# Kernel optimization log

Hardware: AMD Instinct MI355X
Metric: run time of the kernel (lower is better)

Reference implementation:

```python
import jax, jax.numpy as jnp
import numpy as np
from jax import lax

EPS = 1e-5
ENC_CH = [3, 64, 128, 256, 512]
DEC_CH = [512, 256, 128, 64, 3]

def setup_inputs() -> dict:
    key = jax.random.key(0)
    ks = iter(jax.random.split(key, 64))
    d = {}
    d['x'] = jax.random.normal(next(ks), (16, 3, 256, 256), jnp.float32)
    for i in range(4):
        ci, co = ENC_CH[i], ENC_CH[i + 1]
        d[f'enc_w{i}'] = jax.random.normal(next(ks), (co, ci, 3, 3), jnp.float32) / np.sqrt(ci * 9.0).astype(np.float32)
        d[f'enc_b{i}'] = jnp.zeros((co,), jnp.float32)
        d[f'enc_g{i}'] = jnp.ones((co,), jnp.float32)
        d[f'enc_be{i}'] = jnp.zeros((co,), jnp.float32)
    for i in range(4):
        ci, co = DEC_CH[i], DEC_CH[i + 1]
        # torch ConvTranspose2d weight layout: (in, out, kh, kw)
        d[f'dec_w{i}'] = jax.random.normal(next(ks), (ci, co, 3, 3), jnp.float32) / np.sqrt(ci * 9.0).astype(np.float32)
        d[f'dec_b{i}'] = jnp.zeros((co,), jnp.float32)
        d[f'dec_g{i}'] = jnp.ones((co,), jnp.float32)
        d[f'dec_be{i}'] = jnp.zeros((co,), jnp.float32)
    n_emb = 2048
    d['emb'] = jax.random.uniform(next(ks), (n_emb, 512), jnp.float32, minval=-1.0 / n_emb, maxval=1.0 / n_emb)
    return d

def _bn(x, g, b):
    # training-mode batchnorm (biased variance over N,H,W), matching nn.BatchNorm2d default state
    m = jnp.mean(x, (0, 2, 3), keepdims=True)
    v = jnp.mean((x - m) ** 2, (0, 2, 3), keepdims=True)
    return g[None, :, None, None] * (x - m) * lax.rsqrt(v + EPS) + b[None, :, None, None]

def _enc_block(x, w, b, g, be):
    y = lax.conv_general_dilated(x, w, (2, 2), ((1, 1), (1, 1)), dimension_numbers=('NCHW', 'OIHW', 'NCHW'))
    y = y + b[None, :, None, None]
    return jax.nn.gelu(_bn(y, g, be), approximate=False)

def _dec_block(x, w, b, g, be):
    # ConvTranspose2d(k=3, s=2, p=1, output_padding=1): lhs_dilation=2, pad (1,2), flipped kernel
    w2 = jnp.flip(w, (2, 3)).transpose(1, 0, 2, 3)  # (out, in, 3, 3)
    y = lax.conv_general_dilated(x, w2, (1, 1), ((1, 2), (1, 2)), lhs_dilation=(2, 2), dimension_numbers=('NCHW', 'OIHW', 'NCHW'))
    y = y + b[None, :, None, None]
    return jax.nn.gelu(_bn(y, g, be), approximate=False)

def _forward(x, enc_p, dec_p, emb):
    h = x
    for (w, b, g, be) in enc_p:
        h = _enc_block(h, w, b, g, be)
    # --- VectorQuantizer ---
    B, C, H, W = h.shape
    f = h.transpose(0, 2, 3, 1).reshape(B, H * W, C)  # (b, hw, c)
    # squared distances via expansion (same math as broadcasted diff-sum, minus the 34GB intermediate)
    d2 = jnp.sum(f * f, -1, keepdims=True) - 2.0 * jnp.einsum('bnc,ec->bne', f, emb) + jnp.sum(emb * emb, -1)[None, None, :]
    idx = jnp.argmin(d2, -1)  # (b, hw)
    e = emb[idx]  # (b, hw, c)
    e = e.transpose(0, 2, 1).reshape(B, C, H, W)
    sg = lax.stop_gradient
    loss = jnp.mean((h - sg(e)) ** 2) + 0.25 * jnp.mean((sg(h) - e) ** 2)
    # NOTE: original forward returns x (encoder output), NOT the quantized emb_x — faithful to source
    y = h
    for (w, b, g, be) in dec_p:
        y = _dec_block(y, w, b, g, be)
    return jnp.tanh(y), loss

def reference(x, enc_w0, enc_b0, enc_g0, enc_be0, enc_w1, enc_b1, enc_g1, enc_be1, enc_w2, enc_b2, enc_g2, enc_be2, enc_w3, enc_b3, enc_g3, enc_be3, dec_w0, dec_b0, dec_g0, dec_be0, dec_w1, dec_b1, dec_g1, dec_be1, dec_w2, dec_b2, dec_g2, dec_be2, dec_w3, dec_b3, dec_g3, dec_be3, emb):
    enc_p = [(enc_w0, enc_b0, enc_g0, enc_be0), (enc_w1, enc_b1, enc_g1, enc_be1), (enc_w2, enc_b2, enc_g2, enc_be2), (enc_w3, enc_b3, enc_g3, enc_be3)]
    dec_p = [(dec_w0, dec_b0, dec_g0, dec_be0), (dec_w1, dec_b1, dec_g1, dec_be1), (dec_w2, dec_b2, dec_g2, dec_be2), (dec_w3, dec_b3, dec_g3, dec_be3)]
    return _forward(x, enc_p, dec_p, emb)
```

## Files before the change

kernel.cpp:

```cpp
#include <hip/hip_runtime.h>
#include <math.h>

typedef _Float16 half8 __attribute__((ext_vector_type(8)));
typedef _Float16 half4t __attribute__((ext_vector_type(4)));
typedef float floatx4 __attribute__((ext_vector_type(4)));

struct ConvDesc {
  int HI, WI;
  int CIs;
  int OYs, OXs;
  int SXY;
  int osxy;
  int HO, WO;
  int CO_pad, CO_real, CO_store;
  int nclass;
  int py[4], px[4], nt[4];
  int tt[4][9], tdy[4][9], tdx[4][9];
};

#define STAT_SLOTS 16

template<int BM, int BN>
__global__ __launch_bounds__(256) void conv_gemm(
    const _Float16* __restrict__ act, const _Float16* __restrict__ wB,
    const float* __restrict__ bias, _Float16* __restrict__ y,
    float* __restrict__ stats, ConvDesc d)
{
  constexpr int WM = BM / 2, WN = BN / 2, FM = WM / 16, FN = WN / 16;
  constexpr int ARPT = BM / 64, BT = BN / 64;
  constexpr int AP = BM * 8 + 8;
  constexpr int ASZ = 4 * AP;
  constexpr int BSZ = BT * 2048;
  __shared__ __align__(16) _Float16 As[2 * ASZ];
  __shared__ __align__(16) _Float16 Bs[2 * BSZ];

  const int tid = threadIdx.x;
  const int cls = blockIdx.z;
  const int m0 = blockIdx.x * BM, n0 = blockIdx.y * BN;
  const int q = tid & 3, r0 = tid >> 2;

  int aih[ARPT], aiw[ARPT], abase[ARPT];
  #pragma unroll
  for (int i = 0; i < ARPT; i++) {
    int p = m0 + r0 + i * 64;
    int n  = p >> (d.OYs + d.OXs);
    int oy = (p >> d.OXs) & ((1 << d.OYs) - 1);
    int ox = p & ((1 << d.OXs) - 1);
    aih[i] = oy * d.SXY;
    aiw[i] = ox * d.SXY;
    abase[i] = n * d.HI;
  }

  floatx4 acc[FM][FN] = {};
  const int wv = tid >> 6, lane = tid & 63;
  const int wm = wv >> 1, wn = wv & 1;
  const int fr = lane >> 4, fc = lane & 15;
  const int c5s = d.CIs - 5;
  const int c5m = (1 << c5s) - 1;
  const int kiters = d.nt[cls] << c5s;

  auto stageK = [&](int kk, int buf) {
    int ti = kk >> c5s, c5 = kk & c5m;
    int dy = d.tdy[cls][ti], dx = d.tdx[cls][ti];
    int kt0 = d.tt[cls][ti] << c5s;
    int c0 = c5 << 5;
    #pragma unroll
    for (int i = 0; i < ARPT; i++) {
      int ih = aih[i] + dy, iw = aiw[i] + dx;
      half8 v = {};
      if ((unsigned)ih < (unsigned)d.HI && (unsigned)iw < (unsigned)d.WI)
        v = *(const half8*)(act + ((((size_t)(abase[i] + ih)) * d.WI + iw) << d.CIs) + c0 + q * 8);
      *(half8*)(As + buf * ASZ + q * AP + (r0 + i * 64) * 8) = v;
    }
    #pragma unroll
    for (int j = 0; j < BT; j++) {
      const _Float16* src = wB + (size_t)((kt0 + c5) * (d.CO_pad >> 6) + (n0 >> 6) + j) * 2048 + tid * 8;
      *(half8*)(Bs + buf * BSZ + j * 2048 + tid * 8) = *(const half8*)src;
    }
  };

  stageK(0, 0);
  for (int kk = 0; kk < kiters; kk++) {
    __syncthreads();
    if (kk + 1 < kiters) stageK(kk + 1, (kk + 1) & 1);
    const int buf = kk & 1;
    half8 af[FM], bf[FN];
    #pragma unroll
    for (int a = 0; a < FM; a++)
      af[a] = *(const half8*)(As + buf * ASZ + fr * AP + (wm * WM + a * 16 + fc) * 8);
    #pragma unroll
    for (int b = 0; b < FN; b++) {
      int col = wn * WN + b * 16 + fc;
      bf[b] = *(const half8*)(Bs + buf * BSZ + (col >> 6) * 2048 + fr * 512 + (col & 63) * 8);
    }
    #pragma unroll
    for (int a = 0; a < FM; a++)
      #pragma unroll
      for (int b = 0; b < FN; b++)
        acc[a][b] = __builtin_amdgcn_mfma_f32_16x16x32_f16(af[a], bf[b], acc[a][b], 0, 0, 0);
  }

  float bv[FN];
  int colg[FN];
  #pragma unroll
  for (int b = 0; b < FN; b++) {
    int col = n0 + wn * WN + b * 16 + fc;
    colg[b] = col;
    bv[b] = (col < d.CO_real) ? bias[col] : 0.f;
  }
  float ssum[FN] = {}, ssq[FN] = {};
  const int pyc = d.py[cls], pxc = d.px[cls];
  #pragma unroll
  for (int a = 0; a < FM; a++) {
    #pragma unroll
    for (int rr = 0; rr < 4; rr++) {
      int m = m0 + wm * WM + a * 16 + fr * 4 + rr;
      int n  = m >> (d.OYs + d.OXs);
      int oy = (m >> d.OXs) & ((1 << d.OYs) - 1);
      int ox = m & ((1 << d.OXs) - 1);
      size_t opix = ((size_t)(n * d.HO + oy * d.osxy + pyc)) * d.WO + ox * d.osxy + pxc;
      _Float16* dst = y + opix * d.CO_store;
      #pragma unroll
      for (int b = 0; b < FN; b++) {
        float val = acc[a][b][rr] + bv[b];
        if (colg[b] < d.CO_store) dst[colg[b]] = (_Float16)val;
        ssum[b] += val; ssq[b] += val * val;
      }
    }
  }

  __syncthreads();
  float2* red = (float2*)As;
  #pragma unroll
  for (int b = 0; b < FN; b++)
    red[(wn * WN + b * 16 + fc) * 8 + wm * 4 + fr] = make_float2(ssum[b], ssq[b]);
  __syncthreads();
  if (tid < BN) {
    float s = 0.f, qv = 0.f;
    #pragma unroll
    for (int g2 = 0; g2 < 8; g2++) { float2 v = red[tid * 8 + g2]; s += v.x; qv += v.y; }
    int slot = (blockIdx.x + blockIdx.z) & (STAT_SLOTS - 1);
    float* sp = stats + ((size_t)(n0 + tid) * STAT_SLOTS + slot) * 2;
    atomicAdd(sp, s); atomicAdd(sp + 1, qv);
  }
}

__global__ __launch_bounds__(256) void dec3_fused(
    const _Float16* __restrict__ act, const _Float16* __restrict__ wB,
    const float* __restrict__ bias, _Float16* __restrict__ y,
    float* __restrict__ stats)
{
  __shared__ __align__(16) _Float16 As[4 * 3168];
  __shared__ __align__(16) _Float16 Bs[9216];
  const int tid = threadIdx.x;
  const int n = blockIdx.x >> 6;
  const int y0 = (blockIdx.x & 63) << 1;
  const int wv = tid >> 6, lane = tid & 63;
  const int fr = lane >> 4, fc = lane & 15;

  for (int i = tid; i < 1152; i += 256)
    *(half8*)(Bs + i * 8) = *(const half8*)(wB + i * 8);

  floatx4 acc[4][4] = {};

  for (int c5 = 0; c5 < 2; c5++) {
    __syncthreads();
    for (int i = tid; i < 1584; i += 256) {
      int slot = i >> 2, q = i & 3;
      int prow = slot / 132, pcol = slot - prow * 132;
      int row = y0 + prow;
      half8 v = {};
      if (row < 128 && pcol < 128)
        v = *(const half8*)(act + (((size_t)(n * 128 + row)) * 128 + pcol) * 64 + c5 * 32 + q * 8);
      *(half8*)(As + q * 3168 + slot * 8) = v;
    }
    __syncthreads();
    #pragma unroll
    for (int t = 0; t < 9; t++) {
      const int ky = t / 3, kx = t % 3;
      const int dy = (ky == 0) ? 1 : 0, dx = (kx == 0) ? 1 : 0;
      const int cls = ((ky + 1) & 1) * 2 + ((kx + 1) & 1);
      half8 bf = *(const half8*)(Bs + (t * 2 + c5) * 512 + fr * 128 + fc * 8);
      #pragma unroll
      for (int a = 0; a < 4; a++) {
        int m = wv * 64 + a * 16 + fc;
        int r = m >> 7, xx = m & 127;
        half8 af = *(const half8*)(As + fr * 3168 + ((r + dy) * 132 + xx + dx) * 8);
        acc[cls][a] = __builtin_amdgcn_mfma_f32_16x16x32_f16(af, bf, acc[cls][a], 0, 0, 0);
      }
    }
  }

  float bv = (fc < 3) ? bias[fc] : 0.f;
  float s4 = 0.f, q4 = 0.f;
  if (fc < 4) {
    #pragma unroll
    for (int cls = 0; cls < 4; cls++) {
      int py = cls >> 1, px = cls & 1;
      #pragma unroll
      for (int a = 0; a < 4; a++) {
        #pragma unroll
        for (int rr = 0; rr < 4; rr++) {
          int m = wv * 64 + a * 16 + fr * 4 + rr;
          int r = m >> 7, xx = m & 127;
          size_t opix = ((size_t)(n * 256 + (y0 + r) * 2 + py)) * 256 + xx * 2 + px;
          float val = acc[cls][a][rr] + bv;
          y[opix * 4 + fc] = (_Float16)val;
          s4 += val; q4 += val * val;
        }
      }
    }
  }
  __syncthreads();
  float2* red = (float2*)As;
  if (fc < 4) red[fc * 16 + wv * 4 + fr] = make_float2(s4, q4);
  __syncthreads();
  if (tid < 4) {
    float s = 0.f, qv = 0.f;
    #pragma unroll
    for (int g2 = 0; g2 < 16; g2++) { float2 v = red[tid * 16 + g2]; s += v.x; qv += v.y; }
    int slot = blockIdx.x & (STAT_SLOTS - 1);
    float* sp = stats + ((size_t)tid * STAT_SLOTS + slot) * 2;
    atomicAdd(sp, s); atomicAdd(sp + 1, qv);
  }
}

__global__ __launch_bounds__(256) void vq_gemm(const _Float16* __restrict__ h,
    const _Float16* __restrict__ embB, const float* __restrict__ ee,
    float* __restrict__ minval, int* __restrict__ minidx)
{
  __shared__ char smem[32768];
  _Float16* As = (_Float16*)smem;
  _Float16* Bs = (_Float16*)(smem + 8448);
  const int tid = threadIdx.x;
  const int m0 = blockIdx.x * 128, n0 = blockIdx.y * 128;
  const int q = tid & 3, r0 = tid >> 2;
  floatx4 acc[4][4] = {};
  const int wv = tid >> 6, lane = tid & 63;
  const int wm = wv >> 1, wn = wv & 1;
  const int fr = lane >> 4, fc = lane & 15;

  for (int c5 = 0; c5 < 16; c5++) {
    #pragma unroll
    for (int i = 0; i < 2; i++) {
      half8 v = *(const half8*)(h + (size_t)(m0 + r0 + i * 64) * 512 + c5 * 32 + q * 8);
      *(half8*)(As + q * 1032 + (r0 + i * 64) * 8) = v;
    }
    #pragma unroll
    for (int j = 0; j < 2; j++)
      *(half8*)(Bs + j * 2048 + tid * 8) =
          *(const half8*)(embB + (size_t)(c5 * 32 + (n0 >> 6) + j) * 2048 + tid * 8);
    __syncthreads();
    half8 af[4], bf[4];
    #pragma unroll
    for (int a = 0; a < 4; a++)
      af[a] = *(const half8*)(As + fr * 1032 + (wm * 64 + a * 16 + fc) * 8);
    #pragma unroll
    for (int b = 0; b < 4; b++) {
      int col = wn * 64 + b * 16 + fc;
      bf[b] = *(const half8*)(Bs + (col >> 6) * 2048 + fr * 512 + (col & 63) * 8);
    }
    #pragma unroll
    for (int a = 0; a < 4; a++)
      #pragma unroll
      for (int b = 0; b < 4; b++)
        acc[a][b] = __builtin_amdgcn_mfma_f32_16x16x32_f16(af[a], bf[b], acc[a][b], 0, 0, 0);
    __syncthreads();
  }

  float* sval = (float*)smem;
  int*   sidx = (int*)(smem + 16384);
  #pragma unroll
  for (int a = 0; a < 4; a++) {
    #pragma unroll
    for (int rr = 0; rr < 4; rr++) {
      int rb = wm * 64 + a * 16 + fr * 4 + rr;
      float best = 1e30f; int bi = 0;
      #pragma unroll
      for (int b = 0; b < 4; b++) {
        int e = n0 + wn * 64 + b * 16 + fc;
        float s = ee[e] - 2.f * acc[a][b][rr];
        if (s < best) { best = s; bi = e; }
      }
      sval[rb * 32 + wn * 16 + fc] = best;
      sidx[rb * 32 + wn * 16 + fc] = bi;
    }
  }
  __syncthreads();
  if (tid < 128) {
    float best = sval[tid * 32]; int bi = sidx[tid * 32];
    for (int t = 1; t < 32; t++) {
      float v = sval[tid * 32 + t]; int ix = sidx[tid * 32 + t];
      if (v < best || (v == best && ix < bi)) { best = v; bi = ix; }
    }
    minval[(size_t)(m0 + tid) * 16 + blockIdx.y] = best;
    minidx[(size_t)(m0 + tid) * 16 + blockIdx.y] = bi;
  }
}

__global__ __launch_bounds__(256) void vq_finalize(const _Float16* __restrict__ h,
    const float* __restrict__ emb, const float* __restrict__ minval,
    const int* __restrict__ minidx, float* __restrict__ lossacc)
{
  const int tid = threadIdx.x;
  const int g = tid >> 4, l = tid & 15;
  const int v = blockIdx.x * 16 + g;
  float val = minval[(size_t)v * 16 + l];
  int   idx = minidx[(size_t)v * 16 + l];
  #pragma unroll
  for (int o = 8; o > 0; o >>= 1) {
    float v2 = __shfl_down(val, o, 16);
    int   i2 = __shfl_down(idx, o, 16);
    if (v2 < val || (v2 == val && i2 < idx)) { val = v2; idx = i2; }
  }
  idx = __shfl(idx, 0, 16);
  float s = 0.f;
  #pragma unroll
  for (int j = 0; j < 32; j++) {
    int c = l + 16 * j;
    float f = (float)h[(size_t)v * 512 + c];
    float e = emb[(size_t)idx * 512 + c];
    float dd = f - e;
    s += dd * dd;
  }
  #pragma unroll
  for (int o = 8; o > 0; o >>= 1) s += __shfl_down(s, o, 16);
  if (l == 0) atomicAdd(lossacc, s);
}

__global__ __launch_bounds__(256) void bn_apply_inline(_Float16* __restrict__ y,
    const float2* __restrict__ stats, const float* __restrict__ g,
    const float* __restrict__ be, int Cs, int n8, float invM)
{
  const int C = 1 << Cs;
  __shared__ float scs[512], shs[512];
  for (int c = threadIdx.x; c < C; c += 256) {
    float s = 0.f, qv = 0.f;
    #pragma unroll
    for (int t = 0; t < STAT_SLOTS; t++) { float2 v = stats[c * STAT_SLOTS + t]; s += v.x; qv += v.y; }
    float m = s * invM, var = qv * invM - m * m;
    float sc = g[c] * rsqrtf(var + 1e-5f);
    scs[c] = sc; shs[c] = be[c] - m * sc;
  }
  __syncthreads();
  int i = blockIdx.x * 256 + threadIdx.x;
  if (i >= n8) return;
  int c0 = (i << 3) & (C - 1);
  half8 v = *(half8*)(y + (size_t)i * 8);
  half8 o;
  #pragma unroll
  for (int j = 0; j < 8; j++) {
    float x = (float)v[j] * scs[c0 + j] + shs[c0 + j];
    o[j] = (_Float16)(0.5f * x * (1.f + erff(x * 0.70710678118654752f)));
  }
  *(half8*)(y + (size_t)i * 8) = o;
}

__global__ __launch_bounds__(256) void bn_final_inline(const _Float16* __restrict__ y,
    float* __restrict__ out, const float2* __restrict__ stats,
    const float* __restrict__ g, const float* __restrict__ be,
    const float* __restrict__ lossacc)
{
  __shared__ float scs[4], shs[4];
  if (threadIdx.x < 3) {
    int c = threadIdx.x;
    float s = 0.f, qv = 0.f;
    #pragma unroll
    for (int t = 0; t < STAT_SLOTS; t++) { float2 v = stats[c * STAT_SLOTS + t]; s += v.x; qv += v.y; }
    const float invM = 1.f / 1048576.f;
    float m = s * invM, var = qv * invM - m * m;
    float sc = g[c] * rsqrtf(var + 1e-5f);
    scs[c] = sc; shs[c] = be[c] - m * sc;
  }
  __syncthreads();
  int p = blockIdx.x * 256 + threadIdx.x;
  int n = p >> 16, hw = p & 65535;
  half4t v = *(const half4t*)(y + (size_t)p * 4);
  #pragma unroll
  for (int c = 0; c < 3; c++) {
    float x = (float)v[c] * scs[c] + shs[c];
    float gg = 0.5f * x * (1.f + erff(x * 0.70710678118654752f));
    out[(size_t)(n * 3 + c) * 65536 + hw] = tanhf(gg);
  }
  if (p == 0) out[3145728] = lossacc[0] * (1.25f / 2097152.0f);
}

__global__ __launch_bounds__(256) void im2col_enc0(const float* __restrict__ x,
                                                   _Float16* __restrict__ xp)
{
  int p = blockIdx.x * 256 + threadIdx.x;
  int n = p >> 14, oy = (p >> 7) & 127, ox = p & 127;
  const float* xb = x + (size_t)n * 3 * 65536;
  _Float16 v[32];
  #pragma unroll
  for (int k = 27; k < 32; k++) v[k] = (_Float16)0.f;
  #pragma unroll
  for (int tap = 0; tap < 9; tap++) {
    int kh = tap / 3, kw = tap - kh * 3;
    int ih = 2 * oy - 1 + kh, iw = 2 * ox - 1 + kw;
    bool ok = ((unsigned)ih < 256u) && ((unsigned)iw < 256u);
    #pragma unroll
    for (int c = 0; c < 3; c++)
      v[tap * 3 + c] = ok ? (_Float16)xb[(size_t)c * 65536 + ih * 256 + iw] : (_Float16)0.f;
  }
  _Float16* dst = xp + (size_t)p * 32;
  #pragma unroll
  for (int j = 0; j < 4; j++) *(half8*)(dst + j * 8) = *(half8*)(v + j * 8);
}

__global__ void wtrans0(const float* __restrict__ w, _Float16* __restrict__ wB)
{
  int idx = blockIdx.x * 256 + threadIdx.x;
  if (idx >= 2048) return;
  int k = idx >> 6, co = idx & 63;
  int tap = k / 3, c = k - tap * 3;
  float v = (k < 27) ? w[((size_t)co * 3 + c) * 9 + tap] : 0.f;
  int kg = (k >> 3) & 3, kj = k & 7;
  wB[kg * 512 + co * 8 + kj] = (_Float16)v;
}

__global__ void wtrans_n16_dec3(const float* __restrict__ w, _Float16* __restrict__ wB)
{
  int idx = blockIdx.x * 256 + threadIdx.x;
  if (idx >= 9216) return;
  int k = idx >> 4, co = idx & 15;
  int tap = k >> 6, ci = k & 63;
  float v = 0.f;
  if (co < 3) v = w[((size_t)ci * 3 + co) * 9 + tap];
  int kt = k >> 5, kg = (k >> 3) & 3, kj = k & 7;
  wB[(size_t)kt * 512 + kg * 128 + co * 8 + kj] = (_Float16)v;
}

__global__ __launch_bounds__(256) void wtrans(const float* __restrict__ w,
    _Float16* __restrict__ wB, int CIs, int CI_real, int COs, int CO_real, int is_dec)
{
  int idx = blockIdx.x * 256 + threadIdx.x;
  int CO_pad = 1 << COs;
  int K = 9 << CIs;
  if (idx >= K * CO_pad) return;
  int k = idx >> COs, co = idx & (CO_pad - 1);
  int tap = k >> CIs, ci = k & ((1 << CIs) - 1);
  int kh = tap / 3, kw = tap - kh * 3;
  float v = 0.f;
  if (ci < CI_real && co < CO_real)
    v = is_dec ? w[(((size_t)ci * CO_real + co) * 3 + kh) * 3 + kw]
               : w[(((size_t)co * CI_real + ci) * 3 + kh) * 3 + kw];
  int kt = k >> 5, kg = (k >> 3) & 3, kj = k & 7, jt = co >> 6, cc = co & 63;
  wB[(size_t)(kt * (CO_pad >> 6) + jt) * 2048 + kg * 512 + cc * 8 + kj] = (_Float16)v;
}

__global__ __launch_bounds__(256) void embtrans(const float* __restrict__ emb,
                                                _Float16* __restrict__ embB)
{
  int idx = blockIdx.x * 256 + threadIdx.x;
  int k = idx >> 11, e = idx & 2047;
  float v = emb[(size_t)e * 512 + k];
  int kt = k >> 5, kg = (k >> 3) & 3, kj = k & 7, jt = e >> 6, cc = e & 63;
  embB[(size_t)(kt * 32 + jt) * 2048 + kg * 512 + cc * 8 + kj] = (_Float16)v;
}

__global__ __launch_bounds__(256) void emb_norms(const float* __restrict__ emb,
                                                 float* __restrict__ ee)
{
  const int wv = threadIdx.x >> 6, lane = threadIdx.x & 63;
  const int e = blockIdx.x * 4 + wv;
  float s = 0.f;
  #pragma unroll
  for (int j = 0; j < 8; j++) { float v = emb[(size_t)e * 512 + lane + j * 64]; s += v * v; }
  for (int o = 32; o > 0; o >>= 1) s += __shfl_down(s, o);
  if (lane == 0) ee[e] = s;
}

__global__ __launch_bounds__(256) void zero_stats(float* __restrict__ p, int n)
{
  int i = blockIdx.x * 256 + threadIdx.x;
  if (i < n) p[i] = 0.f;
}

static ConvDesc enc_desc(int HI, int WI, int CIs, int CO) {
  ConvDesc d = {};
  d.HI = HI; d.WI = WI; d.CIs = CIs;
  int HO = HI / 2, WO = WI / 2;
  d.OYs = __builtin_ctz(HO); d.OXs = __builtin_ctz(WO);
  d.SXY = 2; d.osxy = 1; d.HO = HO; d.WO = WO;
  d.CO_pad = CO; d.CO_real = CO; d.CO_store = CO;
  d.nclass = 1; d.py[0] = 0; d.px[0] = 0; d.nt[0] = 9;
  for (int t = 0; t < 9; t++) { d.tt[0][t] = t; d.tdy[0][t] = t / 3 - 1; d.tdx[0][t] = t % 3 - 1; }
  return d;
}

static ConvDesc dec_desc(int HI, int WI, int CIs, int CO_pad, int CO_real, int CO_store) {
  ConvDesc d = {};
  d.HI = HI; d.WI = WI; d.CIs = CIs;
  d.OYs = __builtin_ctz(HI); d.OXs = __builtin_ctz(WI);
  d.SXY = 1; d.osxy = 2; d.HO = 2 * HI; d.WO = 2 * WI;
  d.CO_pad = CO_pad; d.CO_real = CO_real; d.CO_store = CO_store;
  d.nclass = 4;
  int kys[2][2] = {{1, -1}, {0, 2}}, dis[2][2] = {{0, -1}, {1, 0}}, cnt[2] = {1, 2};
  for (int py = 0; py < 2; py++)
    for (int px = 0; px < 2; px++) {
      int c = py * 2 + px; d.py[c] = py; d.px[c] = px;
      int m = 0;
      for (int a = 0; a < cnt[py]; a++)
        for (int b = 0; b < cnt[px]; b++) {
          d.tt[c][m] = kys[py][a] * 3 + kys[px][b];
          d.tdy[c][m] = dis[py][a]; d.tdx[c][m] = dis[px][b]; m++;
        }
      d.nt[c] = m;
    }
  return d;
}

extern "C" void kernel_launch(void* const* d_in, const int* in_sizes, int n_in,
                              void* d_out, int out_size, void* d_ws, size_t ws_size,
                              hipStream_t stream)
{
  const float* x = (const float*)d_in[0];
  const float *ew[4], *ebi[4], *eg[4], *ebe[4];
  const float *dw[4], *dbi[4], *dg[4], *dbe[4];
  for (int i = 0; i < 4; i++) {
    ew[i]  = (const float*)d_in[1 + 4 * i];
    ebi[i] = (const float*)d_in[2 + 4 * i];
    eg[i]  = (const float*)d_in[3 + 4 * i];
    ebe[i] = (const float*)d_in[4 + 4 * i];
    dw[i]  = (const float*)d_in[17 + 4 * i];
    dbi[i] = (const float*)d_in[18 + 4 * i];
    dg[i]  = (const float*)d_in[19 + 4 * i];
    dbe[i] = (const float*)d_in[20 + 4 * i];
  }
  const float* emb = (const float*)d_in[33];
  float* out = (float*)d_out;
  _Float16* wsh = (_Float16*)d_ws;

  _Float16* bufA = wsh;
  _Float16* xp   = wsh;
  _Float16* bufB = wsh + 33554432;
  size_t wboff = 50331648;
  _Float16* wbE[4], *wbD[4];
  size_t wbsz[8] = {18432, 73728, 294912, 1179648, 1179648, 294912, 73728, 36864};
  for (int i = 0; i < 4; i++) { wbE[i] = wsh + wboff; wboff += wbsz[i]; }
  for (int i = 0; i < 4; i++) { wbD[i] = wsh + wboff; wboff += wbsz[4 + i]; }
  _Float16* embB = wsh + wboff;
  float* f32 = (float*)(wsh + 54532096);
  float* statsAll = f32;
  float* lossacc  = f32 + 131072;
  float* ee       = f32 + 131080;
  float* minval   = f32 + 133128;
  int*   minidx   = (int*)(f32 + 198664);
  auto statsL = [&](int i) { return statsAll + (size_t)i * 16384; };

  zero_stats<<<513, 256, 0, stream>>>(statsAll, 131073);
  im2col_enc0<<<1024, 256, 0, stream>>>(x, xp);
  wtrans0<<<8, 256, 0, stream>>>(ew[0], wbE[0]);
  wtrans<<<288, 256, 0, stream>>>(ew[1], wbE[1], 6, 64, 7, 128, 0);
  wtrans<<<1152, 256, 0, stream>>>(ew[2], wbE[2], 7, 128, 8, 256, 0);
  wtrans<<<4608, 256, 0, stream>>>(ew[3], wbE[3], 8, 256, 9, 512, 0);
  wtrans<<<4608, 256, 0, stream>>>(dw[0], wbD[0], 9, 512, 8, 256, 1);
  wtrans<<<1152, 256, 0, stream>>>(dw[1], wbD[1], 8, 256, 7, 128, 1);
  wtrans<<<288, 256, 0, stream>>>(dw[2], wbD[2], 7, 128, 6, 64, 1);
  wtrans_n16_dec3<<<36, 256, 0, stream>>>(dw[3], wbD[3]);
  embtrans<<<4096, 256, 0, stream>>>(emb, embB);
  emb_norms<<<512, 256, 0, stream>>>(emb, ee);

  {
    ConvDesc d = {};
    d.HI = 512; d.WI = 512; d.CIs = 5; d.OYs = 9; d.OXs = 9; d.SXY = 1; d.osxy = 1;
    d.HO = 512; d.WO = 512; d.CO_pad = 64; d.CO_real = 64; d.CO_store = 64;
    d.nclass = 1; d.nt[0] = 1;
    conv_gemm<128, 64><<<dim3(2048, 1, 1), 256, 0, stream>>>(xp, wbE[0], ebi[0], bufB, statsL(0), d);
    bn_apply_inline<<<8192, 256, 0, stream>>>(bufB, (const float2*)statsL(0), eg[0], ebe[0], 6, 2097152, 1.f / 262144.f);
  }
  {
    ConvDesc d = enc_desc(128, 128, 6, 128);
    conv_gemm<128, 128><<<dim3(512, 1, 1), 256, 0, stream>>>(bufB, wbE[1], ebi[1], bufA, statsL(1), d);
    bn_apply_inline<<<4096, 256, 0, stream>>>(bufA, (const float2*)statsL(1), eg[1], ebe[1], 7, 1048576, 1.f / 65536.f);
  }
  {
    ConvDesc d = enc_desc(64, 64, 7, 256);
    conv_gemm<128, 64><<<dim3(128, 4, 1), 256, 0, stream>>>(bufA, wbE[2], ebi[2], bufB, statsL(2), d);
    bn_apply_inline<<<2048, 256, 0, stream>>>(bufB, (const float2*)statsL(2), eg[2], ebe[2], 8, 524288, 1.f / 16384.f);
  }
  {
    ConvDesc d = enc_desc(32, 32, 8, 512);
    conv_gemm<64, 64><<<dim3(64, 8, 1), 256, 0, stream>>>(bufB, wbE[3], ebi[3], bufA, statsL(3), d);
    bn_apply_inline<<<1024, 256, 0, stream>>>(bufA, (const float2*)statsL(3), eg[3], ebe[3], 9, 262144, 1.f / 4096.f);
  }
  _Float16* h = bufA;

  vq_gemm<<<dim3(32, 16), 256, 0, stream>>>(h, embB, ee, minval, minidx);
  vq_finalize<<<256, 256, 0, stream>>>(h, emb, minval, minidx, lossacc);

  {
    ConvDesc d = dec_desc(16, 16, 9, 256, 256, 256);
    conv_gemm<64, 64><<<dim3(64, 4, 4), 256, 0, stream>>>(h, wbD[0], dbi[0], bufB, statsL(4), d);
    bn_apply_inline<<<2048, 256, 0, stream>>>(bufB, (const float2*)statsL(4), dg[0], dbe[0], 8, 524288, 1.f / 16384.f);
  }
  {
    ConvDesc d = dec_desc(32, 32, 8, 128, 128, 128);
    conv_gemm<128, 128><<<dim3(128, 1, 4), 256, 0, stream>>>(bufB, wbD[1], dbi[1], bufA, statsL(5), d);
    bn_apply_inline<<<4096, 256, 0, stream>>>(bufA, (const float2*)statsL(5), dg[1], dbe[1], 7, 1048576, 1.f / 65536.f);
  }
  {
    ConvDesc d = dec_desc(64, 64, 7, 64, 64, 64);
    conv_gemm<128, 64><<<dim3(512, 1, 4), 256, 0, stream>>>(bufA, wbD[2], dbi[2], bufB, statsL(6), d);
    bn_apply_inline<<<8192, 256, 0, stream>>>(bufB, (const float2*)statsL(6), dg[2], dbe[2], 6, 2097152, 1.f / 262144.f);
  }
  {
    dec3_fused<<<1024, 256, 0, stream>>>(bufB, wbD[3], dbi[3], bufA, statsL(7));
    bn_final_inline<<<4096, 256, 0, stream>>>(bufA, out, (const float2*)statsL(7), dg[3], dbe[3], lossacc);
  }
}
```

Before: 696.0 us.

## Merge prep kernels into one launch and add fused dec2 transposed-conv kernel

Replaces the twelve preprocessing launches (stat zeroing, im2col, weight and embedding transposes, embedding norms) with a single prep_all kernel that dispatches on block index, cutting launch overhead. It also replaces the generic 4-class conv_gemm for decoder layer 2 with a dedicated dec2_fused kernel. Each block of that kernel loads one input row pair into LDS once and computes all four output parity classes from it, reusing the input tile across classes. The risks are branch divergence in the merged prep kernel and lower occupancy from the large LDS weight buffer in dec2_fused.

```diff
diff --git a/kernel.cpp b/kernel.cpp
--- a/kernel.cpp
+++ b/kernel.cpp
@@ -145,6 +145,87 @@
   }
 }
 
+__global__ __launch_bounds__(256) void dec2_fused(
+    const _Float16* __restrict__ act, const _Float16* __restrict__ wB,
+    const float* __restrict__ bias, _Float16* __restrict__ y,
+    float* __restrict__ stats)
+{
+  __shared__ __align__(16) _Float16 As[4 * 1056];
+  __shared__ __align__(16) _Float16 Bs[18432];
+  const int tid = threadIdx.x;
+  const int n = blockIdx.x >> 6;
+  const int R = blockIdx.x & 63;
+  const int wv = tid >> 6, lane = tid & 63;
+  const int fr = lane >> 4, fc = lane & 15;
+
+  floatx4 acc[4][4] = {};
+
+  for (int c5 = 0; c5 < 4; c5++) {
+    __syncthreads();
+    for (int i = tid; i < 528; i += 256) {
+      int slot = i >> 2, q = i & 3;
+      int hr = slot / 66, hc = slot - hr * 66;
+      int grow = R + hr;
+      half8 v = {};
+      if (grow < 64 && hc < 64)
+        v = *(const half8*)(act + (((size_t)(n * 64 + grow)) * 64 + hc) * 128 + c5 * 32 + q * 8);
+      *(half8*)(As + q * 1056 + slot * 8) = v;
+    }
+    #pragma unroll
+    for (int t = 0; t < 9; t++)
+      *(half8*)(Bs + t * 2048 + tid * 8) =
+          *(const half8*)(wB + (size_t)(t * 4 + c5) * 2048 + tid * 8);
+    __syncthreads();
+    #pragma unroll
+    for (int t = 0; t < 9; t++) {
+      const int ky = t / 3, kx = t % 3;
+      const int dy = (ky == 0) ? 1 : 0, dx = (kx == 0) ? 1 : 0;
+      const int cls = ((ky + 1) & 1) * 2 + ((kx + 1) & 1);
+      half8 af = *(const half8*)(As + fr * 1056 + (dy * 66 + wv * 16 + fc + dx) * 8);
+      #pragma unroll
+      for (int b = 0; b < 4; b++) {
+        half8 bf = *(const half8*)(Bs + t * 2048 + fr * 512 + (b * 16 + fc) * 8);
+        acc[cls][b] = __builtin_amdgcn_mfma_f32_16x16x32_f16(af, bf, acc[cls][b], 0, 0, 0);
+      }
+    }
+  }
+
+  float bv[4];
+  #pragma unroll
+  for (int b = 0; b < 4; b++) bv[b] = bias[b * 16 + fc];
+  float ssum[4] = {}, ssq[4] = {};
+  #pragma unroll
+  for (int cls = 0; cls < 4; cls++) {
+    int py = cls >> 1, px = cls & 1;
+    int orow = 2 * R + py;
+    #pragma unroll
+    for (int b = 0; b < 4; b++) {
+      #pragma unroll
+      for (int rr = 0; rr < 4; rr++) {
+        int ipx = wv * 16 + fr * 4 + rr;
+        size_t opix = ((size_t)(n * 128 + orow)) * 128 + 2 * ipx + px;
+        float val = acc[cls][b][rr] + bv[b];
+        y[opix * 64 + b * 16 + fc] = (_Float16)val;
+        ssum[b] += val; ssq[b] += val * val;
+      }
+    }
+  }
+  __syncthreads();
+  float2* red = (float2*)As;
+  #pragma unroll
+  for (int b = 0; b < 4; b++)
+    red[(b * 16 + fc) * 16 + wv * 4 + fr] = make_float2(ssum[b], ssq[b]);
+  __syncthreads();
+  if (tid < 64) {
+    float s = 0.f, qv = 0.f;
+    #pragma unroll
+    for (int g2 = 0; g2 < 16; g2++) { float2 v = red[tid * 16 + g2]; s += v.x; qv += v.y; }
+    int slot = blockIdx.x & (STAT_SLOTS - 1);
+    float* sp = stats + ((size_t)tid * STAT_SLOTS + slot) * 2;
+    atomicAdd(sp, s); atomicAdd(sp + 1, qv);
+  }
+}
+
 __global__ __launch_bounds__(256) void dec3_fused(
     const _Float16* __restrict__ act, const _Float16* __restrict__ wB,
     const float* __restrict__ bias, _Float16* __restrict__ y,
@@ -385,59 +466,17 @@
   if (p == 0) out[3145728] = lossacc[0] * (1.25f / 2097152.0f);
 }
 
-__global__ __launch_bounds__(256) void im2col_enc0(const float* __restrict__ x,
-                                                   _Float16* __restrict__ xp)
-{
-  int p = blockIdx.x * 256 + threadIdx.x;
-  int n = p >> 14, oy = (p >> 7) & 127, ox = p & 127;
-  const float* xb = x + (size_t)n * 3 * 65536;
-  _Float16 v[32];
-  #pragma unroll
-  for (int k = 27; k < 32; k++) v[k] = (_Float16)0.f;
-  #pragma unroll
-  for (int tap = 0; tap < 9; tap++) {
-    int kh = tap / 3, kw = tap - kh * 3;
-    int ih = 2 * oy - 1 + kh, iw = 2 * ox - 1 + kw;
-    bool ok = ((unsigned)ih < 256u) && ((unsigned)iw < 256u);
-    #pragma unroll
-    for (int c = 0; c < 3; c++)
-      v[tap * 3 + c] = ok ? (_Float16)xb[(size_t)c * 65536 + ih * 256 + iw] : (_Float16)0.f;
-  }
-  _Float16* dst = xp + (size_t)p * 32;
-  #pragma unroll
-  for (int j = 0; j < 4; j++) *(half8*)(dst + j * 8) = *(half8*)(v + j * 8);
-}
-
-__global__ void wtrans0(const float* __restrict__ w, _Float16* __restrict__ wB)
-{
-  int idx = blockIdx.x * 256 + threadIdx.x;
-  if (idx >= 2048) return;
-  int k = idx >> 6, co = idx & 63;
-  int tap = k / 3, c = k - tap * 3;
-  float v = (k < 27) ? w[((size_t)co * 3 + c) * 9 + tap] : 0.f;
-  int kg = (k >> 3) & 3, kj = k & 7;
-  wB[kg * 512 + co * 8 + kj] = (_Float16)v;
-}
-
-__global__ void wtrans_n16_dec3(const float* __restrict__ w, _Float16* __restrict__ wB)
-{
-  int idx = blockIdx.x * 256 + threadIdx.x;
-  if (idx >= 9216) return;
-  int k = idx >> 4, co = idx & 15;
-  int tap = k >> 6, ci = k & 63;
-  float v = 0.f;
-  if (co < 3) v = w[((size_t)ci * 3 + co) * 9 + tap];
-  int kt = k >> 5, kg = (k >> 3) & 3, kj = k & 7;
-  wB[(size_t)kt * 512 + kg * 128 + co * 8 + kj] = (_Float16)v;
-}
-
-__global__ __launch_bounds__(256) void wtrans(const float* __restrict__ w,
-    _Float16* __restrict__ wB, int CIs, int CI_real, int COs, int CO_real, int is_dec)
-{
-  int idx = blockIdx.x * 256 + threadIdx.x;
+struct PrepPtrs {
+  const float *ew0, *ew1, *ew2, *ew3, *dw0, *dw1, *dw2, *dw3, *emb, *x;
+  _Float16 *wbE0, *wbE1, *wbE2, *wbE3, *wbD0, *wbD1, *wbD2, *wbD3, *embB, *xp;
+  float *ee, *stats;
+};
+
+__device__ __forceinline__ void wtrans_g(const float* __restrict__ w,
+    _Float16* __restrict__ wB, int CIs, int CI_real, int COs, int CO_real,
+    int is_dec, int idx)
+{
   int CO_pad = 1 << COs;
-  int K = 9 << CIs;
-  if (idx >= K * CO_pad) return;
   int k = idx >> COs, co = idx & (CO_pad - 1);
   int tap = k >> CIs, ci = k & ((1 << CIs) - 1);
   int kh = tap / 3, kw = tap - kh * 3;
@@ -449,32 +488,74 @@
   wB[(size_t)(kt * (CO_pad >> 6) + jt) * 2048 + kg * 512 + cc * 8 + kj] = (_Float16)v;
 }
 
-__global__ __launch_bounds__(256) void embtrans(const float* __restrict__ emb,
-                                                _Float16* __restrict__ embB)
-{
-  int idx = blockIdx.x * 256 + threadIdx.x;
-  int k = idx >> 11, e = idx & 2047;
-  float v = emb[(size_t)e * 512 + k];
-  int kt = k >> 5, kg = (k >> 3) & 3, kj = k & 7, jt = e >> 6, cc = e & 63;
-  embB[(size_t)(kt * 32 + jt) * 2048 + kg * 512 + cc * 8 + kj] = (_Float16)v;
-}
-
-__global__ __launch_bounds__(256) void emb_norms(const float* __restrict__ emb,
-                                                 float* __restrict__ ee)
-{
-  const int wv = threadIdx.x >> 6, lane = threadIdx.x & 63;
-  const int e = blockIdx.x * 4 + wv;
-  float s = 0.f;
-  #pragma unroll
-  for (int j = 0; j < 8; j++) { float v = emb[(size_t)e * 512 + lane + j * 64]; s += v * v; }
-  for (int o = 32; o > 0; o >>= 1) s += __shfl_down(s, o);
-  if (lane == 0) ee[e] = s;
-}
-
-__global__ __launch_bounds__(256) void zero_stats(float* __restrict__ p, int n)
-{
-  int i = blockIdx.x * 256 + threadIdx.x;
-  if (i < n) p[i] = 0.f;
+__global__ __launch_bounds__(256) void prep_all(PrepPtrs P)
+{
+  const int b = blockIdx.x;
+  const int tid = threadIdx.x;
+  if (b < 8) {
+    int idx = b * 256 + tid;
+    int k = idx >> 6, co = idx & 63;
+    int tap = k / 3, c = k - tap * 3;
+    float v = (k < 27) ? P.ew0[((size_t)co * 3 + c) * 9 + tap] : 0.f;
+    int kg = (k >> 3) & 3, kj = k & 7;
+    P.wbE0[kg * 512 + co * 8 + kj] = (_Float16)v;
+  } else if (b < 296) {
+    wtrans_g(P.ew1, P.wbE1, 6, 64, 7, 128, 0, (b - 8) * 256 + tid);
+  } else if (b < 1448) {
+    wtrans_g(P.ew2, P.wbE2, 7, 128, 8, 256, 0, (b - 296) * 256 + tid);
+  } else if (b < 6056) {
+    wtrans_g(P.ew3, P.wbE3, 8, 256, 9, 512, 0, (b - 1448) * 256 + tid);
+  } else if (b < 10664) {
+    wtrans_g(P.dw0, P.wbD0, 9, 512, 8, 256, 1, (b - 6056) * 256 + tid);
+  } else if (b < 11816) {
+    wtrans_g(P.dw1, P.wbD1, 8, 256, 7, 128, 1, (b - 10664) * 256 + tid);
+  } else if (b < 12104) {
+    wtrans_g(P.dw2, P.wbD2, 7, 128, 6, 64, 1, (b - 11816) * 256 + tid);
+  } else if (b < 12140) {
+    int idx = (b - 12104) * 256 + tid;
+    int k = idx >> 4, co = idx & 15;
+    int tap = k >> 6, ci = k & 63;
+    float v = 0.f;
+    if (co < 3) v = P.dw3[((size_t)ci * 3 + co) * 9 + tap];
+    int kt = k >> 5, kg = (k >> 3) & 3, kj = k & 7;
+    P.wbD3[(size_t)kt * 512 + kg * 128 + co * 8 + kj] = (_Float16)v;
+  } else if (b < 16236) {
+    int idx = (b - 12140) * 256 + tid;
+    int k = idx >> 11, e = idx & 2047;
+    float v = P.emb[(size_t)e * 512 + k];
+    int kt = k >> 5, kg = (k >> 3) & 3, kj = k & 7, jt = e >> 6, cc = e & 63;
+    P.embB[(size_t)(kt * 32 + jt) * 2048 + kg * 512 + cc * 8 + kj] = (_Float16)v;
+  } else if (b < 16749) {
+    int i = (b - 16236) * 256 + tid;
+    if (i < 131073) P.stats[i] = 0.f;
+  } else if (b < 17261) {
+    int wv = tid >> 6, lane = tid & 63;
+    int e = (b - 16749) * 4 + wv;
+    float s = 0.f;
+    #pragma unroll
+    for (int j = 0; j < 8; j++) { float v = P.emb[(size_t)e * 512 + lane + j * 64]; s += v * v; }
+    for (int o = 32; o > 0; o >>= 1) s += __shfl_down(s, o);
+    if (lane == 0) P.ee[e] = s;
+  } else {
+    int p = (b - 17261) * 256 + tid;
+    int n = p >> 14, oy = (p >> 7) & 127, ox = p & 127;
+    const float* xb = P.x + (size_t)n * 3 * 65536;
+    _Float16 v[32];
+    #pragma unroll
+    for (int k = 27; k < 32; k++) v[k] = (_Float16)0.f;
+    #pragma unroll
+    for (int tap = 0; tap < 9; tap++) {
+      int kh = tap / 3, kw = tap - kh * 3;
+      int ih = 2 * oy - 1 + kh, iw = 2 * ox - 1 + kw;
+      bool ok = ((unsigned)ih < 256u) && ((unsigned)iw < 256u);
+      #pragma unroll
+      for (int c = 0; c < 3; c++)
+        v[tap * 3 + c] = ok ? (_Float16)xb[(size_t)c * 65536 + ih * 256 + iw] : (_Float16)0.f;
+    }
+    _Float16* dst = P.xp + (size_t)p * 32;
+    #pragma unroll
+    for (int j = 0; j < 4; j++) *(half8*)(dst + j * 8) = *(half8*)(v + j * 8);
+  }
 }
 
 static ConvDesc enc_desc(int HI, int WI, int CIs, int CO) {
@@ -549,18 +630,14 @@
   int*   minidx   = (int*)(f32 + 198664);
   auto statsL = [&](int i) { return statsAll + (size_t)i * 16384; };
 
-  zero_stats<<<513, 256, 0, stream>>>(statsAll, 131073);
-  im2col_enc0<<<1024, 256, 0, stream>>>(x, xp);
-  wtrans0<<<8, 256, 0, stream>>>(ew[0], wbE[0]);
-  wtrans<<<288, 256, 0, stream>>>(ew[1], wbE[1], 6, 64, 7, 128, 0);
-  wtrans<<<1152, 256, 0, stream>>>(ew[2], wbE[2], 7, 128, 8, 256, 0);
-  wtrans<<<4608, 256, 0, stream>>>(ew[3], wbE[3], 8, 256, 9, 512, 0);
-  wtrans<<<4608, 256, 0, stream>>>(dw[0], wbD[0], 9, 512, 8, 256, 1);
-  wtrans<<<1152, 256, 0, stream>>>(dw[1], wbD[1], 8, 256, 7, 128, 1);
-  wtrans<<<288, 256, 0, stream>>>(dw[2], wbD[2], 7, 128, 6, 64, 1);
-  wtrans_n16_dec3<<<36, 256, 0, stream>>>(dw[3], wbD[3]);
-  embtrans<<<4096, 256, 0, stream>>>(emb, embB);
-  emb_norms<<<512, 256, 0, stream>>>(emb, ee);
+  PrepPtrs P;
+  P.ew0 = ew[0]; P.ew1 = ew[1]; P.ew2 = ew[2]; P.ew3 = ew[3];
+  P.dw0 = dw[0]; P.dw1 = dw[1]; P.dw2 = dw[2]; P.dw3 = dw[3];
+  P.emb = emb; P.x = x;
+  P.wbE0 = wbE[0]; P.wbE1 = wbE[1]; P.wbE2 = wbE[2]; P.wbE3 = wbE[3];
+  P.wbD0 = wbD[0]; P.wbD1 = wbD[1]; P.wbD2 = wbD[2]; P.wbD3 = wbD[3];
+  P.embB = embB; P.xp = xp; P.ee = ee; P.stats = statsAll;
+  prep_all<<<18285, 256, 0, stream>>>(P);
 
   {
     ConvDesc d = {};
@@ -601,8 +678,7 @@
     bn_apply_inline<<<4096, 256, 0, stream>>>(bufA, (const float2*)statsL(5), dg[1], dbe[1], 7, 1048576, 1.f / 65536.f);
   }
   {
-    ConvDesc d = dec_desc(64, 64, 7, 64, 64, 64);
-    conv_gemm<128, 64><<<dim3(512, 1, 4), 256, 0, stream>>>(bufA, wbD[2], dbi[2], bufB, statsL(6), d);
+    dec2_fused<<<1024, 256, 0, stream>>>(bufA, wbD[2], dbi[2], bufB, statsL(6));
     bn_apply_inline<<<8192, 256, 0, stream>>>(bufB, (const float2*)statsL(6), dg[2], dbe[2], 6, 2097152, 1.f / 262144.f);
   }
   {
```

Result: faster. 649.8 us (-6.6%).
